# Performance work log

Measured on AMD Instinct MI355X. Metric: run time of the kernel, lower is better.

The kernel has to match this reference:

```python
import jax, jax.numpy as jnp
import numpy as np

D_OUT = 64  # out_embed_size, also the softmax scale base

def setup_inputs() -> dict:
    key = jax.random.key(0)
    kx, kk, kq, kv = jax.random.split(key, 4)
    B, T, C = 8, 2048, 768
    x = jax.random.normal(kx, (B, T, C), dtype=jnp.float32)
    # torch Linear weights are [out, in]; store as [in, out] for x @ W
    s = 1.0 / np.sqrt(C)
    Wk = jax.random.uniform(kk, (C, D_OUT), jnp.float32, -s, s)
    Wq = jax.random.uniform(kq, (C, D_OUT), jnp.float32, -s, s)
    Wv = jax.random.uniform(kv, (C, D_OUT), jnp.float32, -s, s)
    return {"x": x, "Wq": Wq, "Wk": Wk, "Wv": Wv}

def reference(x, Wq, Wk, Wv):
    B, T, C = x.shape
    q = x @ Wq  # [B,T,D]
    k = x @ Wk
    v = x @ Wv
    scale = D_OUT ** -0.5
    qk = jnp.einsum('btd,bsd->bts', q, k) * scale  # [B,T,T]
    causal = jnp.tril(jnp.ones((T, T), dtype=bool))
    qk = jnp.where(causal, qk, -jnp.inf)
    attn = jax.nn.softmax(qk, axis=-1)
    # dropout p=0.0 -> identity
    return jnp.einsum('bts,bsd->btd', attn, v)
```

## Files before the change

### kernel.cpp

```cpp
#include <hip/hip_runtime.h>
#include <hip/hip_bf16.h>

#define BB 8
#define TT 2048
#define CC 768
#define DD 64
#define BT (BB * TT)

typedef __attribute__((ext_vector_type(8))) short bf16x8;
typedef __attribute__((ext_vector_type(4))) float f32x4;

__device__ __forceinline__ unsigned short f2b(float f) {
  unsigned u = __builtin_bit_cast(unsigned, f);
  u += 0x7fffu + ((u >> 16) & 1u);
  return (unsigned short)(u >> 16);
}

__global__ __launch_bounds__(256) void wt_kernel(const float* __restrict__ Wq,
                                                 const float* __restrict__ Wk,
                                                 const float* __restrict__ Wv,
                                                 unsigned short* __restrict__ wt) {
  int tid = blockIdx.x * 256 + threadIdx.x;
  if (tid >= 192 * 96) return;
  int k0 = (tid % 96) * 8;
  int c = tid / 96;
  const float* W = (c < 64) ? Wq : (c < 128 ? Wk : Wv);
  int cc = c & 63;
  unsigned short t[8];
#pragma unroll
  for (int e = 0; e < 8; ++e) t[e] = f2b(W[(k0 + e) * 64 + cc]);
  *reinterpret_cast<bf16x8*>(&wt[c * 768 + k0]) = *reinterpret_cast<bf16x8*>(t);
}

__global__ __launch_bounds__(512, 4) void proj_kernel(const float* __restrict__ x,
                                                      const unsigned short* __restrict__ wt,
                                                      unsigned short* __restrict__ qws,
                                                      unsigned short* __restrict__ kws,
                                                      unsigned short* __restrict__ vtws) {
  __shared__ unsigned short xl[32][72];
  __shared__ unsigned short wl[192][72];

  const int tid = threadIdx.x;
  const int wv = tid >> 6;
  const int l = tid & 63;
  const int lo = l & 15, hi = l >> 4;
  const int rg = wv & 1;
  const int cq = wv >> 1;
  const int m0 = blockIdx.x * 32;

  f32x4 acc[3];
#pragma unroll
  for (int i = 0; i < 3; ++i) acc[i] = (f32x4){0.f, 0.f, 0.f, 0.f};

  const int xrow = tid >> 4;
  const int xc4 = (tid & 15) * 4;

  for (int k0 = 0; k0 < 768; k0 += 64) {
    {
      float4 xv = *reinterpret_cast<const float4*>(&x[(size_t)(m0 + xrow) * 768 + k0 + xc4]);
      ushort4 t;
      t.x = f2b(xv.x); t.y = f2b(xv.y); t.z = f2b(xv.z); t.w = f2b(xv.w);
      *reinterpret_cast<ushort4*>(&xl[xrow][xc4]) = t;
    }
#pragma unroll
    for (int it = 0; it < 3; ++it) {
      int ch = tid + it * 512;
      int row = ch >> 3, c8 = (ch & 7) * 8;
      *reinterpret_cast<bf16x8*>(&wl[row][c8]) =
          *reinterpret_cast<const bf16x8*>(&wt[row * 768 + k0 + c8]);
    }
    __syncthreads();

    bf16x8 af0 = *reinterpret_cast<const bf16x8*>(&xl[rg * 16 + lo][hi * 8]);
    bf16x8 af1 = *reinterpret_cast<const bf16x8*>(&xl[rg * 16 + lo][32 + hi * 8]);
#pragma unroll
    for (int ct = 0; ct < 3; ++ct) {
      int cr = cq * 48 + ct * 16 + lo;
      bf16x8 b0 = *reinterpret_cast<const bf16x8*>(&wl[cr][hi * 8]);
      bf16x8 b1 = *reinterpret_cast<const bf16x8*>(&wl[cr][32 + hi * 8]);
      acc[ct] = __builtin_amdgcn_mfma_f32_16x16x32_bf16(af0, b0, acc[ct], 0, 0, 0);
      acc[ct] = __builtin_amdgcn_mfma_f32_16x16x32_bf16(af1, b1, acc[ct], 0, 0, 0);
    }
    __syncthreads();
  }

  const float QS = 0.125f * 1.4426950408889634f;
#pragma unroll
  for (int ct = 0; ct < 3; ++ct) {
    const int c = cq * 48 + ct * 16 + lo;
    const int mat = c >> 6;
    const int cc = c & 63;
#pragma unroll
    for (int r = 0; r < 4; ++r) {
      const int m = m0 + rg * 16 + hi * 4 + r;
      float val = acc[ct][r];
      if (mat == 0) {
        qws[m * 64 + cc] = f2b(val * QS);
      } else if (mat == 1) {
        kws[m * 64 + cc] = f2b(val);
      } else {
        vtws[(size_t)((m >> 11) * 64 + cc) * 2048 + (m & 2047)] = f2b(val);
      }
    }
  }
}

__global__ __launch_bounds__(512, 4) void attn_kernel(const unsigned short* __restrict__ qws,
                                                      const unsigned short* __restrict__ kws,
                                                      const unsigned short* __restrict__ vtws,
                                                      float* __restrict__ out) {
  __shared__ unsigned short Pl[8][16][72];
  __shared__ float Obuf[32][68];
  __shared__ float Ssum[32];

  const int tid = threadIdx.x;
  const int wv = tid >> 6;
  const int l = tid & 63;
  const int lo = l & 15, hi = l >> 4;
  const int rg = wv & 1;
  const int s = wv >> 1;
  const int bx = blockIdx.x;
  const int b = bx & 7;
  const int qt = bx >> 3;
  const int t0 = qt * 32;
  const int nt = (qt >> 1) + 1;

  {
    float* p = &Obuf[0][0];
    for (int i = tid; i < 32 * 68; i += 512) p[i] = 0.f;
    if (tid < 32) Ssum[tid] = 0.f;
  }
  __syncthreads();

  const unsigned short* qb = qws + (size_t)b * TT * DD;
  const unsigned short* kb = kws + (size_t)b * TT * DD;
  const unsigned short* vb = vtws + (size_t)b * DD * TT;

  const int qrow = t0 + rg * 16 + lo;
  bf16x8 qf0 = *reinterpret_cast<const bf16x8*>(&qb[qrow * 64 + hi * 8]);
  bf16x8 qf1 = *reinterpret_cast<const bf16x8*>(&qb[qrow * 64 + 32 + hi * 8]);

  f32x4 Oa[4];
#pragma unroll
  for (int n = 0; n < 4; ++n) Oa[n] = (f32x4){0.f, 0.f, 0.f, 0.f};
  float srow[4] = {0.f, 0.f, 0.f, 0.f};

  for (int j = s; j < nt; j += 4) {
    f32x4 S[4];
#pragma unroll
    for (int n = 0; n < 4; ++n) S[n] = (f32x4){0.f, 0.f, 0.f, 0.f};
    const unsigned short* kt = kb + (size_t)(j * 64) * 64;
#pragma unroll
    for (int n = 0; n < 4; ++n) {
      bf16x8 k0f = *reinterpret_cast<const bf16x8*>(&kt[(n * 16 + lo) * 64 + hi * 8]);
      bf16x8 k1f = *reinterpret_cast<const bf16x8*>(&kt[(n * 16 + lo) * 64 + 32 + hi * 8]);
      S[n] = __builtin_amdgcn_mfma_f32_16x16x32_bf16(qf0, k0f, S[n], 0, 0, 0);
      S[n] = __builtin_amdgcn_mfma_f32_16x16x32_bf16(qf1, k1f, S[n], 0, 0, 0);
    }
    if (j == nt - 1) {
#pragma unroll
      for (int n = 0; n < 4; ++n) {
        int kvg = j * 64 + n * 16 + lo;
#pragma unroll
        for (int r = 0; r < 4; ++r) {
          int qg = t0 + rg * 16 + hi * 4 + r;
          if (kvg > qg) S[n][r] = -1e30f;
        }
      }
    }
#pragma unroll
    for (int n = 0; n < 4; ++n)
#pragma unroll
      for (int r = 0; r < 4; ++r) {
        float p = exp2f(S[n][r]);
        srow[r] += p;
        Pl[wv][hi * 4 + r][n * 16 + lo] = f2b(p);
      }
    bf16x8 pa0 = *reinterpret_cast<const bf16x8*>(&Pl[wv][lo][hi * 8]);
    bf16x8 pa1 = *reinterpret_cast<const bf16x8*>(&Pl[wv][lo][32 + hi * 8]);
    const unsigned short* vt = vb + j * 64;
#pragma unroll
    for (int n = 0; n < 4; ++n) {
      bf16x8 v0 = *reinterpret_cast<const bf16x8*>(&vt[(size_t)(n * 16 + lo) * 2048 + hi * 8]);
      bf16x8 v1 = *reinterpret_cast<const bf16x8*>(&vt[(size_t)(n * 16 + lo) * 2048 + 32 + hi * 8]);
      Oa[n] = __builtin_amdgcn_mfma_f32_16x16x32_bf16(pa0, v0, Oa[n], 0, 0, 0);
      Oa[n] = __builtin_amdgcn_mfma_f32_16x16x32_bf16(pa1, v1, Oa[n], 0, 0, 0);
    }
  }

#pragma unroll
  for (int n = 0; n < 4; ++n)
#pragma unroll
    for (int r = 0; r < 4; ++r)
      atomicAdd(&Obuf[rg * 16 + hi * 4 + r][n * 16 + lo], Oa[n][r]);
#pragma unroll
  for (int r = 0; r < 4; ++r) {
    float v = srow[r];
    v += __shfl_xor(v, 1);
    v += __shfl_xor(v, 2);
    v += __shfl_xor(v, 4);
    v += __shfl_xor(v, 8);
    if (lo == 0) atomicAdd(&Ssum[rg * 16 + hi * 4 + r], v);
  }
  __syncthreads();

  {
    const int row = tid >> 4;
    const int c4 = (tid & 15) * 4;
    const float inv = 1.0f / Ssum[row];
    float4 o;
    o.x = Obuf[row][c4 + 0] * inv;
    o.y = Obuf[row][c4 + 1] * inv;
    o.z = Obuf[row][c4 + 2] * inv;
    o.w = Obuf[row][c4 + 3] * inv;
    *reinterpret_cast<float4*>(&out[((size_t)b * TT + t0 + row) * 64 + c4]) = o;
  }
}

extern "C" void kernel_launch(void* const* d_in, const int* in_sizes, int n_in,
                              void* d_out, int out_size, void* d_ws, size_t ws_size,
                              hipStream_t stream) {
  const float* x = (const float*)d_in[0];
  const float* Wq = (const float*)d_in[1];
  const float* Wk = (const float*)d_in[2];
  const float* Wv = (const float*)d_in[3];
  float* out = (float*)d_out;

  char* ws = (char*)d_ws;
  unsigned short* qws = (unsigned short*)(ws);
  unsigned short* kws = (unsigned short*)(ws + (size_t)2 * 1024 * 1024);
  unsigned short* vtws = (unsigned short*)(ws + (size_t)4 * 1024 * 1024);
  unsigned short* wt = (unsigned short*)(ws + (size_t)6 * 1024 * 1024);

  hipLaunchKernelGGL(wt_kernel, dim3(72), dim3(256), 0, stream, Wq, Wk, Wv, wt);
  hipLaunchKernelGGL(proj_kernel, dim3(BT / 32), dim3(512), 0, stream, x, wt, qws, kws, vtws);
  hipLaunchKernelGGL(attn_kernel, dim3(512), dim3(512), 0, stream, qws, kws, vtws, out);
}
```

Before: 166.1 us.

## Double-buffer projection and attention via async LDS loads with XOR swizzle and balanced tiles

The projection kernel now stages fp32 x and bf16 weights into double-buffered, XOR-swizzled LDS using global_load_lds, converting x to bf16 at fragment load time, so the next tile's loads overlap the current MFMAs. The attention kernel is restructured into 256-thread blocks that each process two 16-row query tiles (u and 127-u) for causal load balance. K/V tiles of 128 keys are cooperatively staged into swizzled, double-buffered LDS, and each wave takes a 32-key slice. This removes redundant per-wave global K/V fetches and load imbalance, at the cost of more LDS, extra barriers and a smaller per-block query tile.

Result: faster. 145.6 us (-12.4%).

```diff
diff --git a/kernel.cpp b/kernel.cpp
--- a/kernel.cpp
+++ b/kernel.cpp
@@ -14,6 +14,18 @@
   unsigned u = __builtin_bit_cast(unsigned, f);
   u += 0x7fffu + ((u >> 16) & 1u);
   return (unsigned short)(u >> 16);
+}
+
+__device__ __forceinline__ bf16x8 pack8(float4 a, float4 b) {
+  unsigned short t[8] = {f2b(a.x), f2b(a.y), f2b(a.z), f2b(a.w),
+                         f2b(b.x), f2b(b.y), f2b(b.z), f2b(b.w)};
+  return *reinterpret_cast<bf16x8*>(t);
+}
+
+__device__ __forceinline__ void gl16(const void* g, void* l) {
+  __builtin_amdgcn_global_load_lds(
+      (const __attribute__((address_space(1))) unsigned int*)g,
+      (__attribute__((address_space(3))) unsigned int*)l, 16, 0, 0);
 }
 
 __global__ __launch_bounds__(256) void wt_kernel(const float* __restrict__ Wq,
@@ -32,13 +44,13 @@
   *reinterpret_cast<bf16x8*>(&wt[c * 768 + k0]) = *reinterpret_cast<bf16x8*>(t);
 }
 
-__global__ __launch_bounds__(512, 4) void proj_kernel(const float* __restrict__ x,
+__global__ __launch_bounds__(512, 2) void proj_kernel(const float* __restrict__ x,
                                                       const unsigned short* __restrict__ wt,
                                                       unsigned short* __restrict__ qws,
                                                       unsigned short* __restrict__ kws,
                                                       unsigned short* __restrict__ vtws) {
-  __shared__ unsigned short xl[32][72];
-  __shared__ unsigned short wl[192][72];
+  __shared__ __align__(16) float xl[2][32 * 64];
+  __shared__ __align__(16) unsigned short wl[2][192 * 64];
 
   const int tid = threadIdx.x;
   const int wv = tid >> 6;
@@ -48,40 +60,55 @@
   const int cq = wv >> 1;
   const int m0 = blockIdx.x * 32;
 
+  const int xrow = tid >> 4;
+  const int xcs = ((tid & 15) ^ (xrow & 7)) * 4;
+  const float* xsrc = x + (size_t)(m0 + xrow) * 768 + xcs;
+  const int xdst = (tid & ~63) * 4;
+
   f32x4 acc[3];
 #pragma unroll
   for (int i = 0; i < 3; ++i) acc[i] = (f32x4){0.f, 0.f, 0.f, 0.f};
 
-  const int xrow = tid >> 4;
-  const int xc4 = (tid & 15) * 4;
-
-  for (int k0 = 0; k0 < 768; k0 += 64) {
-    {
-      float4 xv = *reinterpret_cast<const float4*>(&x[(size_t)(m0 + xrow) * 768 + k0 + xc4]);
-      ushort4 t;
-      t.x = f2b(xv.x); t.y = f2b(xv.y); t.z = f2b(xv.z); t.w = f2b(xv.w);
-      *reinterpret_cast<ushort4*>(&xl[xrow][xc4]) = t;
-    }
+  auto stage = [&](int buf, int k0) {
+    gl16(xsrc + k0, &xl[buf][xdst]);
 #pragma unroll
     for (int it = 0; it < 3; ++it) {
       int ch = tid + it * 512;
-      int row = ch >> 3, c8 = (ch & 7) * 8;
-      *reinterpret_cast<bf16x8*>(&wl[row][c8]) =
-          *reinterpret_cast<const bf16x8*>(&wt[row * 768 + k0 + c8]);
-    }
-    __syncthreads();
-
-    bf16x8 af0 = *reinterpret_cast<const bf16x8*>(&xl[rg * 16 + lo][hi * 8]);
-    bf16x8 af1 = *reinterpret_cast<const bf16x8*>(&xl[rg * 16 + lo][32 + hi * 8]);
+      int row = ch >> 3;
+      int c = ((ch & 7) ^ (row & 7)) * 8;
+      gl16(wt + row * 768 + k0 + c, &wl[buf][(ch & ~63) * 8]);
+    }
+  };
+
+  stage(0, 0);
+  __syncthreads();
+
+  const int arow = rg * 16 + lo;
+  const int ax = arow & 7;
+  int buf = 0;
+#pragma unroll
+  for (int step = 0; step < 12; ++step) {
+    if (step < 11) stage(buf ^ 1, (step + 1) * 64);
+
+    const float* xb = xl[buf];
+    const unsigned short* wb = wl[buf];
+    float4 a0 = *reinterpret_cast<const float4*>(&xb[arow * 64 + ((hi * 2 + 0) ^ ax) * 4]);
+    float4 a1 = *reinterpret_cast<const float4*>(&xb[arow * 64 + ((hi * 2 + 1) ^ ax) * 4]);
+    float4 a2 = *reinterpret_cast<const float4*>(&xb[arow * 64 + ((8 + hi * 2 + 0) ^ ax) * 4]);
+    float4 a3 = *reinterpret_cast<const float4*>(&xb[arow * 64 + ((8 + hi * 2 + 1) ^ ax) * 4]);
+    bf16x8 af0 = pack8(a0, a1);
+    bf16x8 af1 = pack8(a2, a3);
 #pragma unroll
     for (int ct = 0; ct < 3; ++ct) {
       int cr = cq * 48 + ct * 16 + lo;
-      bf16x8 b0 = *reinterpret_cast<const bf16x8*>(&wl[cr][hi * 8]);
-      bf16x8 b1 = *reinterpret_cast<const bf16x8*>(&wl[cr][32 + hi * 8]);
+      int cx = cr & 7;
+      bf16x8 b0 = *reinterpret_cast<const bf16x8*>(&wb[cr * 64 + ((hi) ^ cx) * 8]);
+      bf16x8 b1 = *reinterpret_cast<const bf16x8*>(&wb[cr * 64 + ((4 + hi) ^ cx) * 8]);
       acc[ct] = __builtin_amdgcn_mfma_f32_16x16x32_bf16(af0, b0, acc[ct], 0, 0, 0);
       acc[ct] = __builtin_amdgcn_mfma_f32_16x16x32_bf16(af1, b1, acc[ct], 0, 0, 0);
     }
     __syncthreads();
+    buf ^= 1;
   }
 
   const float QS = 0.125f * 1.4426950408889634f;
@@ -105,115 +132,147 @@
   }
 }
 
-__global__ __launch_bounds__(512, 4) void attn_kernel(const unsigned short* __restrict__ qws,
+__global__ __launch_bounds__(256, 2) void attn_kernel(const unsigned short* __restrict__ qws,
                                                       const unsigned short* __restrict__ kws,
                                                       const unsigned short* __restrict__ vtws,
                                                       float* __restrict__ out) {
-  __shared__ unsigned short Pl[8][16][72];
-  __shared__ float Obuf[32][68];
-  __shared__ float Ssum[32];
+  __shared__ __align__(16) unsigned short Kl[2][128 * 64];
+  __shared__ __align__(16) unsigned short Vl[2][64 * 128];
+  __shared__ __align__(16) unsigned short Pl[4][16 * 40];
+  __shared__ float Obuf[16][68];
+  __shared__ float Ssum[16];
 
   const int tid = threadIdx.x;
-  const int wv = tid >> 6;
+  const int s = tid >> 6;
   const int l = tid & 63;
   const int lo = l & 15, hi = l >> 4;
-  const int rg = wv & 1;
-  const int s = wv >> 1;
-  const int bx = blockIdx.x;
-  const int b = bx & 7;
-  const int qt = bx >> 3;
-  const int t0 = qt * 32;
-  const int nt = (qt >> 1) + 1;
-
-  {
-    float* p = &Obuf[0][0];
-    for (int i = tid; i < 32 * 68; i += 512) p[i] = 0.f;
-    if (tid < 32) Ssum[tid] = 0.f;
-  }
-  __syncthreads();
+  const int b = blockIdx.x & 7;
+  const int u0 = blockIdx.x >> 3;
 
   const unsigned short* qb = qws + (size_t)b * TT * DD;
   const unsigned short* kb = kws + (size_t)b * TT * DD;
   const unsigned short* vb = vtws + (size_t)b * DD * TT;
-
-  const int qrow = t0 + rg * 16 + lo;
-  bf16x8 qf0 = *reinterpret_cast<const bf16x8*>(&qb[qrow * 64 + hi * 8]);
-  bf16x8 qf1 = *reinterpret_cast<const bf16x8*>(&qb[qrow * 64 + 32 + hi * 8]);
-
-  f32x4 Oa[4];
-#pragma unroll
-  for (int n = 0; n < 4; ++n) Oa[n] = (f32x4){0.f, 0.f, 0.f, 0.f};
-  float srow[4] = {0.f, 0.f, 0.f, 0.f};
-
-  for (int j = s; j < nt; j += 4) {
-    f32x4 S[4];
-#pragma unroll
-    for (int n = 0; n < 4; ++n) S[n] = (f32x4){0.f, 0.f, 0.f, 0.f};
-    const unsigned short* kt = kb + (size_t)(j * 64) * 64;
-#pragma unroll
-    for (int n = 0; n < 4; ++n) {
-      bf16x8 k0f = *reinterpret_cast<const bf16x8*>(&kt[(n * 16 + lo) * 64 + hi * 8]);
-      bf16x8 k1f = *reinterpret_cast<const bf16x8*>(&kt[(n * 16 + lo) * 64 + 32 + hi * 8]);
-      S[n] = __builtin_amdgcn_mfma_f32_16x16x32_bf16(qf0, k0f, S[n], 0, 0, 0);
-      S[n] = __builtin_amdgcn_mfma_f32_16x16x32_bf16(qf1, k1f, S[n], 0, 0, 0);
-    }
-    if (j == nt - 1) {
+  unsigned short* Plw = &Pl[s][0];
+
+  auto stage = [&](int buf, int kv0) {
+#pragma unroll
+    for (int it = 0; it < 4; ++it) {
+      int ch = tid + it * 256;
+      int kr = ch >> 3;
+      int kc = ((ch & 7) ^ (kr & 7)) * 8;
+      gl16(kb + (size_t)(kv0 + kr) * 64 + kc, &Kl[buf][(ch & ~63) * 8]);
+      int vd = ch >> 4;
+      int vc = ((ch & 15) ^ (vd & 7)) * 8;
+      gl16(vb + (size_t)vd * 2048 + kv0 + vc, &Vl[buf][(ch & ~63) * 8]);
+    }
+  };
+
+  for (int phase = 0; phase < 2; ++phase) {
+    const int u = phase ? (127 - u0) : u0;
+    const int t0 = u * 16;
+    const int nt = (u >> 3) + 1;
+
+    __syncthreads();
+    for (int i = tid; i < 16 * 68; i += 256) (&Obuf[0][0])[i] = 0.f;
+    if (tid < 16) Ssum[tid] = 0.f;
+
+    bf16x8 qf0 = *reinterpret_cast<const bf16x8*>(&qb[(t0 + lo) * 64 + hi * 8]);
+    bf16x8 qf1 = *reinterpret_cast<const bf16x8*>(&qb[(t0 + lo) * 64 + 32 + hi * 8]);
+
+    f32x4 Oa[4];
+#pragma unroll
+    for (int n = 0; n < 4; ++n) Oa[n] = (f32x4){0.f, 0.f, 0.f, 0.f};
+    float srow[4] = {0.f, 0.f, 0.f, 0.f};
+
+    stage(0, 0);
+    __syncthreads();
+
+    int buf = 0;
+    for (int j = 0; j < nt; ++j) {
+      if (j + 1 < nt) stage(buf ^ 1, (j + 1) * 128);
+
+      const unsigned short* Kb = &Kl[buf][0];
+      const unsigned short* Vb = &Vl[buf][0];
+
+      f32x4 S0 = (f32x4){0.f, 0.f, 0.f, 0.f};
+      f32x4 S1 = (f32x4){0.f, 0.f, 0.f, 0.f};
+      {
+        int key = s * 32 + lo;
+        int kx = key & 7;
+        bf16x8 k0f = *reinterpret_cast<const bf16x8*>(&Kb[key * 64 + ((hi) ^ kx) * 8]);
+        bf16x8 k1f = *reinterpret_cast<const bf16x8*>(&Kb[key * 64 + ((4 + hi) ^ kx) * 8]);
+        S0 = __builtin_amdgcn_mfma_f32_16x16x32_bf16(qf0, k0f, S0, 0, 0, 0);
+        S0 = __builtin_amdgcn_mfma_f32_16x16x32_bf16(qf1, k1f, S0, 0, 0, 0);
+      }
+      {
+        int key = s * 32 + 16 + lo;
+        int kx = key & 7;
+        bf16x8 k0f = *reinterpret_cast<const bf16x8*>(&Kb[key * 64 + ((hi) ^ kx) * 8]);
+        bf16x8 k1f = *reinterpret_cast<const bf16x8*>(&Kb[key * 64 + ((4 + hi) ^ kx) * 8]);
+        S1 = __builtin_amdgcn_mfma_f32_16x16x32_bf16(qf0, k0f, S1, 0, 0, 0);
+        S1 = __builtin_amdgcn_mfma_f32_16x16x32_bf16(qf1, k1f, S1, 0, 0, 0);
+      }
+
+      if (j == nt - 1) {
+        const int kg0 = j * 128 + s * 32 + lo;
+        const int kg1 = kg0 + 16;
+#pragma unroll
+        for (int r = 0; r < 4; ++r) {
+          int qg = t0 + hi * 4 + r;
+          if (kg0 > qg) S0[r] = -1e30f;
+          if (kg1 > qg) S1[r] = -1e30f;
+        }
+      }
+
+#pragma unroll
+      for (int r = 0; r < 4; ++r) {
+        float p0 = exp2f(S0[r]);
+        float p1 = exp2f(S1[r]);
+        srow[r] += p0 + p1;
+        Plw[(hi * 4 + r) * 40 + lo] = f2b(p0);
+        Plw[(hi * 4 + r) * 40 + 16 + lo] = f2b(p1);
+      }
+      bf16x8 pa = *reinterpret_cast<const bf16x8*>(&Plw[lo * 40 + hi * 8]);
+
 #pragma unroll
       for (int n = 0; n < 4; ++n) {
-        int kvg = j * 64 + n * 16 + lo;
-#pragma unroll
-        for (int r = 0; r < 4; ++r) {
-          int qg = t0 + rg * 16 + hi * 4 + r;
-          if (kvg > qg) S[n][r] = -1e30f;
-        }
-      }
-    }
+        int d = n * 16 + lo;
+        int dx = d & 7;
+        bf16x8 vf = *reinterpret_cast<const bf16x8*>(&Vb[d * 128 + ((s * 4 + hi) ^ dx) * 8]);
+        Oa[n] = __builtin_amdgcn_mfma_f32_16x16x32_bf16(pa, vf, Oa[n], 0, 0, 0);
+      }
+
+      __syncthreads();
+      buf ^= 1;
+    }
+
 #pragma unroll
     for (int n = 0; n < 4; ++n)
 #pragma unroll
-      for (int r = 0; r < 4; ++r) {
-        float p = exp2f(S[n][r]);
-        srow[r] += p;
-        Pl[wv][hi * 4 + r][n * 16 + lo] = f2b(p);
-      }
-    bf16x8 pa0 = *reinterpret_cast<const bf16x8*>(&Pl[wv][lo][hi * 8]);
-    bf16x8 pa1 = *reinterpret_cast<const bf16x8*>(&Pl[wv][lo][32 + hi * 8]);
-    const unsigned short* vt = vb + j * 64;
-#pragma unroll
-    for (int n = 0; n < 4; ++n) {
-      bf16x8 v0 = *reinterpret_cast<const bf16x8*>(&vt[(size_t)(n * 16 + lo) * 2048 + hi * 8]);
-      bf16x8 v1 = *reinterpret_cast<const bf16x8*>(&vt[(size_t)(n * 16 + lo) * 2048 + 32 + hi * 8]);
-      Oa[n] = __builtin_amdgcn_mfma_f32_16x16x32_bf16(pa0, v0, Oa[n], 0, 0, 0);
-      Oa[n] = __builtin_amdgcn_mfma_f32_16x16x32_bf16(pa1, v1, Oa[n], 0, 0, 0);
-    }
-  }
-
-#pragma unroll
-  for (int n = 0; n < 4; ++n)
-#pragma unroll
-    for (int r = 0; r < 4; ++r)
-      atomicAdd(&Obuf[rg * 16 + hi * 4 + r][n * 16 + lo], Oa[n][r]);
-#pragma unroll
-  for (int r = 0; r < 4; ++r) {
-    float v = srow[r];
-    v += __shfl_xor(v, 1);
-    v += __shfl_xor(v, 2);
-    v += __shfl_xor(v, 4);
-    v += __shfl_xor(v, 8);
-    if (lo == 0) atomicAdd(&Ssum[rg * 16 + hi * 4 + r], v);
-  }
-  __syncthreads();
-
-  {
-    const int row = tid >> 4;
-    const int c4 = (tid & 15) * 4;
-    const float inv = 1.0f / Ssum[row];
-    float4 o;
-    o.x = Obuf[row][c4 + 0] * inv;
-    o.y = Obuf[row][c4 + 1] * inv;
-    o.z = Obuf[row][c4 + 2] * inv;
-    o.w = Obuf[row][c4 + 3] * inv;
-    *reinterpret_cast<float4*>(&out[((size_t)b * TT + t0 + row) * 64 + c4]) = o;
+      for (int r = 0; r < 4; ++r)
+        atomicAdd(&Obuf[hi * 4 + r][n * 16 + lo], Oa[n][r]);
+#pragma unroll
+    for (int r = 0; r < 4; ++r) {
+      float v = srow[r];
+      v += __shfl_xor(v, 1);
+      v += __shfl_xor(v, 2);
+      v += __shfl_xor(v, 4);
+      v += __shfl_xor(v, 8);
+      if (lo == 0) atomicAdd(&Ssum[hi * 4 + r], v);
+    }
+    __syncthreads();
+
+    {
+      const int row = tid >> 4;
+      const int c4 = (tid & 15) * 4;
+      const float inv = 1.0f / Ssum[row];
+      float4 o;
+      o.x = Obuf[row][c4 + 0] * inv;
+      o.y = Obuf[row][c4 + 1] * inv;
+      o.z = Obuf[row][c4 + 2] * inv;
+      o.w = Obuf[row][c4 + 3] * inv;
+      *reinterpret_cast<float4*>(&out[((size_t)b * TT + t0 + row) * 64 + c4]) = o;
+    }
   }
 }
 
@@ -234,5 +293,5 @@
 
   hipLaunchKernelGGL(wt_kernel, dim3(72), dim3(256), 0, stream, Wq, Wk, Wv, wt);
   hipLaunchKernelGGL(proj_kernel, dim3(BT / 32), dim3(512), 0, stream, x, wt, qws, kws, vtws);
-  hipLaunchKernelGGL(attn_kernel, dim3(512), dim3(512), 0, stream, qws, kws, vtws, out);
-}
+  hipLaunchKernelGGL(attn_kernel, dim3(512), dim3(256), 0, stream, qws, kws, vtws, out);
+}
```
